# Performance work log

Hardware: AMD Instinct MI355X
Metric: run time of the kernel (lower is better)

Reference implementation:

```python
import jax, jax.numpy as jnp
import numpy as np

B, C, H, W = 2, 256, 64, 64
NUM_HEADS = 4
HEAD_DIM = C // NUM_HEADS
N = H * W


def setup_inputs() -> dict:
    key = jax.random.key(0)
    ks = jax.random.split(key, 10)
    x = jax.random.normal(ks[0], (B, C, H, W), dtype=jnp.float32)
    # mostly-True mask; diagonal forced True so every row has a valid key
    m = jax.random.uniform(ks[1], (B, N, N)) > 0.1
    spatial_mask = m | jnp.eye(N, dtype=bool)[None]
    s = 1.0 / np.sqrt(C)
    wq = jax.random.normal(ks[2], (C, C), dtype=jnp.float32) * s
    bq = jnp.zeros((C,), jnp.float32)
    wk = jax.random.normal(ks[3], (C, C), dtype=jnp.float32) * s
    bk = jnp.zeros((C,), jnp.float32)
    wv = jax.random.normal(ks[4], (C, C), dtype=jnp.float32) * s
    bv = jnp.zeros((C,), jnp.float32)
    # torch zero-inits out_proj; use random weights for a non-trivial baseline
    wo = jax.random.normal(ks[5], (C, C), dtype=jnp.float32) * s
    bo = jnp.zeros((C,), jnp.float32)
    return {"x": x, "spatial_mask": spatial_mask, "wq": wq, "bq": bq,
            "wk": wk, "bk": bk, "wv": wv, "bv": bv, "wo": wo, "bo": bo}


def reference(x, spatial_mask, wq, bq, wk, bk, wv, bv, wo, bo):
    b, c, h, w = x.shape
    n = h * w
    nh, hd = NUM_HEADS, HEAD_DIM
    scale = hd ** -0.5
    x_flat = x.reshape(b, c, n).transpose(0, 2, 1)           # [b, n, c]
    q = (x_flat @ wq.T + bq).reshape(b, n, nh, hd).transpose(0, 2, 1, 3)
    k = (x_flat @ wk.T + bk).reshape(b, n, nh, hd).transpose(0, 2, 1, 3)
    v = (x_flat @ wv.T + bv).reshape(b, n, nh, hd).transpose(0, 2, 1, 3)
    logits = jnp.einsum('bhqd,bhkd->bhqk', q, k) * scale      # [b, nh, n, n]
    logits = jnp.where(spatial_mask[:, None], logits, -jnp.inf)
    attn = jax.nn.softmax(logits, axis=-1)                    # dropout = identity (eval)
    out = jnp.einsum('bhqk,bhkd->bhqd', attn, v)              # [b, nh, n, hd]
    out = out.transpose(0, 2, 1, 3).reshape(b, n, c)
    out = out @ wo.T + bo
    return out.transpose(0, 2, 1).reshape(b, c, h, w)
```

## Files before the change

### kernel.cpp

```cpp
#include <hip/hip_runtime.h>
#include <math.h>

namespace {
constexpr int B_    = 2;
constexpr int C_    = 256;
constexpr int NHEAD = 4;
constexpr int HDIM  = 64;
constexpr int NTOK  = 4096;
constexpr float SCALE = 0.125f;
constexpr float LOG2E = 1.44269504f;
}

typedef _Float16 half8  __attribute__((ext_vector_type(8)));
typedef _Float16 half4  __attribute__((ext_vector_type(4)));
typedef __fp16   fp16x2 __attribute__((ext_vector_type(2)));
typedef float    floatx4 __attribute__((ext_vector_type(4)));

__global__ __launch_bounds__(256) void pack_mask(
    const unsigned int* __restrict__ m32, unsigned int* __restrict__ packed)
{
    int c0 = 0, c1 = 0, c2 = 0, c3 = 0;
    #pragma unroll
    for (int i = 0; i < 16; i++) {
        const unsigned int d = m32[i];
        c0 += (d == 0x00000001u);
        c1 += (d == 0x3F803F80u);
        c2 += (d == 0x3F800000u);
        c3 += (d == 0x01010101u);
    }
    int fmt = 1, best = c1;
    if (c0 > best) { best = c0; fmt = 0; }
    if (c2 > best) { best = c2; fmt = 2; }
    if (c3 > best) { best = c3; fmt = 3; }

    const unsigned int W = blockIdx.x * 256 + threadIdx.x;
    unsigned int bits = 0;
    if (fmt == 1) {
        const uint4* p4 = (const uint4*)(m32 + (size_t)W * 16);
        #pragma unroll
        for (int i = 0; i < 4; i++) {
            const uint4 v = p4[i];
            const unsigned int d[4] = { v.x, v.y, v.z, v.w };
            #pragma unroll
            for (int j = 0; j < 4; j++) {
                const int e = i * 8 + j * 2;
                bits |= ((d[j] & 0xFFFFu) ? 1u : 0u) << e;
                bits |= ((d[j] >> 16)     ? 1u : 0u) << (e + 1);
            }
        }
    } else if (fmt != 3) {
        const uint4* p4 = (const uint4*)(m32 + (size_t)W * 32);
        #pragma unroll
        for (int i = 0; i < 8; i++) {
            const uint4 v = p4[i];
            bits |= (v.x ? 1u : 0u) << (i * 4 + 0);
            bits |= (v.y ? 1u : 0u) << (i * 4 + 1);
            bits |= (v.z ? 1u : 0u) << (i * 4 + 2);
            bits |= (v.w ? 1u : 0u) << (i * 4 + 3);
        }
    } else {
        const uint4* p4 = (const uint4*)(m32 + (size_t)W * 8);
        #pragma unroll
        for (int i = 0; i < 2; i++) {
            const uint4 v = p4[i];
            const unsigned int d[4] = { v.x, v.y, v.z, v.w };
            #pragma unroll
            for (int j = 0; j < 4; j++) {
                const int e = (i * 4 + j) * 4;
                bits |= ((d[j] & 0x000000FFu) ? 1u : 0u) << (e + 0);
                bits |= ((d[j] & 0x0000FF00u) ? 1u : 0u) << (e + 1);
                bits |= ((d[j] & 0x00FF0000u) ? 1u : 0u) << (e + 2);
                bits |= ((d[j] & 0xFF000000u) ? 1u : 0u) << (e + 3);
            }
        }
    }
    packed[W] = bits;
}

__global__ __launch_bounds__(256) void qkv_mfma(
    const float* __restrict__ x,
    const float* __restrict__ wq, const float* __restrict__ bq,
    const float* __restrict__ wk, const float* __restrict__ bk,
    const float* __restrict__ wv, const float* __restrict__ bv,
    _Float16* __restrict__ qo, _Float16* __restrict__ ko,
    _Float16* __restrict__ vo)
{
    const int nt = blockIdx.x;
    const int b  = blockIdx.y;
    const int p  = blockIdx.z;

    const float* w; const float* bias;
    if (p == 0)      { w = wq; bias = bq; }
    else if (p == 1) { w = wk; bias = bk; }
    else             { w = wv; bias = bv; }

    const int t    = threadIdx.x;
    const int wid  = t >> 6;
    const int lane = t & 63;
    const int quad = lane >> 4;
    const int l15  = lane & 15;
    const int n0   = nt * 64;

    __shared__ _Float16 xsh[64 * 264];
    __shared__ _Float16 wsh[64 * 72];
    __shared__ _Float16 tbuf[64 * 72];

    const int srow = t >> 2;
    const int sc   = (t & 3) * 16;

    {
        const int cr = t >> 4;
        const int nu = (t & 15) * 4;
        const float* xb = x + (size_t)b * C_ * NTOK;
        #pragma unroll
        for (int cc = 0; cc < 16; cc++) {
            const int cl = cc * 16 + cr;
            const float4 v = *(const float4*)&xb[(size_t)cl * NTOK + n0 + nu];
            xsh[(nu + 0) * 264 + cl] = (_Float16)v.x;
            xsh[(nu + 1) * 264 + cl] = (_Float16)v.y;
            xsh[(nu + 2) * 264 + cl] = (_Float16)v.z;
            xsh[(nu + 3) * 264 + cl] = (_Float16)v.w;
        }
    }

    for (int h = 0; h < NHEAD; h++) {
        const int co0 = h * 64;
        floatx4 acc[4];
        #pragma unroll
        for (int i = 0; i < 4; i++) acc[i] = (floatx4)0.f;

        for (int c0 = 0; c0 < C_; c0 += 64) {
            {
                const float* wr = &w[(size_t)(co0 + srow) * C_ + c0 + sc];
                half8 h0, h1;
                #pragma unroll
                for (int u = 0; u < 2; u++) {
                    const float4 a = *(const float4*)&wr[u * 4];
                    h0[u*4+0]=(_Float16)a.x; h0[u*4+1]=(_Float16)a.y;
                    h0[u*4+2]=(_Float16)a.z; h0[u*4+3]=(_Float16)a.w;
                }
                #pragma unroll
                for (int u = 0; u < 2; u++) {
                    const float4 a = *(const float4*)&wr[8 + u * 4];
                    h1[u*4+0]=(_Float16)a.x; h1[u*4+1]=(_Float16)a.y;
                    h1[u*4+2]=(_Float16)a.z; h1[u*4+3]=(_Float16)a.w;
                }
                *(half8*)&wsh[srow * 72 + sc]     = h0;
                *(half8*)&wsh[srow * 72 + sc + 8] = h1;
            }
            __syncthreads();
            const half8 a0 = *(const half8*)&wsh[(wid * 16 + l15) * 72 + quad * 8];
            const half8 a1 = *(const half8*)&wsh[(wid * 16 + l15) * 72 + 32 + quad * 8];
            #pragma unroll
            for (int nt2 = 0; nt2 < 4; nt2++) {
                const half8 b0 = *(const half8*)&xsh[(nt2 * 16 + l15) * 264 + c0 + quad * 8];
                const half8 b1 = *(const half8*)&xsh[(nt2 * 16 + l15) * 264 + c0 + 32 + quad * 8];
                acc[nt2] = __builtin_amdgcn_mfma_f32_16x16x32_f16(a0, b0, acc[nt2], 0, 0, 0);
                acc[nt2] = __builtin_amdgcn_mfma_f32_16x16x32_f16(a1, b1, acc[nt2], 0, 0, 0);
            }
            __syncthreads();
        }

        const float4 bb4 = *(const float4*)&bias[co0 + wid * 16 + quad * 4];
        const float bb[4] = { bb4.x, bb4.y, bb4.z, bb4.w };

        if (p < 2) {
            const float osc = (p == 0) ? (SCALE * LOG2E) : 1.0f;
            #pragma unroll
            for (int nt2 = 0; nt2 < 4; nt2++) {
                half4 hv;
                #pragma unroll
                for (int i = 0; i < 4; i++)
                    hv[i] = (_Float16)((acc[nt2][i] + bb[i]) * osc);
                *(half4*)&tbuf[(nt2 * 16 + l15) * 72 + wid * 16 + quad * 4] = hv;
            }
            __syncthreads();
            _Float16* dh = (p == 0 ? qo : ko) + (size_t)(b * NHEAD + h) * NTOK * HDIM;
            const half8 o0 = *(const half8*)&tbuf[srow * 72 + sc];
            const half8 o1 = *(const half8*)&tbuf[srow * 72 + sc + 8];
            *(half8*)&dh[(size_t)(n0 + srow) * HDIM + sc]     = o0;
            *(half8*)&dh[(size_t)(n0 + srow) * HDIM + sc + 8] = o1;
        } else {
            #pragma unroll
            for (int nt2 = 0; nt2 < 4; nt2++)
                #pragma unroll
                for (int i = 0; i < 4; i++)
                    tbuf[(wid * 16 + quad * 4 + i) * 72 + nt2 * 16 + l15] =
                        (_Float16)(acc[nt2][i] + bb[i]);
            __syncthreads();
            _Float16* vth = vo + (size_t)(b * NHEAD + h) * HDIM * NTOK;
            const half8 o0 = *(const half8*)&tbuf[srow * 72 + sc];
            const half8 o1 = *(const half8*)&tbuf[srow * 72 + sc + 8];
            *(half8*)&vth[(size_t)srow * NTOK + n0 + sc]     = o0;
            *(half8*)&vth[(size_t)srow * NTOK + n0 + sc + 8] = o1;
        }
        __syncthreads();
    }
}

__global__ __launch_bounds__(512) void attn(
    const _Float16* __restrict__ q, const _Float16* __restrict__ k,
    const _Float16* __restrict__ vt, const unsigned int* __restrict__ mpacked,
    _Float16* __restrict__ ao)
{
    const int b  = blockIdx.z;
    const int h  = blockIdx.y;
    const int q0 = blockIdx.x * 64;
    const int t    = threadIdx.x;
    const int w    = t >> 6;
    const int lane = t & 63;
    const int quad = lane >> 4;
    const int l15  = lane & 15;
    const int half = w >> 2;
    const int w4   = w & 3;
    const int koff = half * (NTOK / 2);

    __shared__ __align__(16) _Float16 ksA[64 * 72];
    __shared__ __align__(16) _Float16 vsA[64 * 72];
    __shared__ __align__(16) _Float16 psA[64 * 72];
    __shared__ __align__(16) _Float16 ksB[64 * 72];
    __shared__ __align__(16) _Float16 vsB[64 * 72];
    __shared__ __align__(16) _Float16 psB[64 * 72];

    _Float16* ksc = half ? ksB : ksA;
    _Float16* vsc = half ? vsB : vsA;
    _Float16* ps  = half ? psB : psA;

    const size_t head_off = (size_t)(b * NHEAD + h) * NTOK * HDIM;
    const _Float16* qb  = q  + head_off;
    const _Float16* kb  = k  + head_off;
    const _Float16* vtb = vt + head_off;
    const unsigned int* mrow = mpacked + (size_t)b * NTOK * 128;

    const int qrow = q0 + w4 * 16 + l15;
    half8 aq0 = *(const half8*)&qb[(size_t)qrow * HDIM + quad * 8];
    half8 aq1 = *(const half8*)&qb[(size_t)qrow * HDIM + 32 + quad * 8];
    const unsigned int* mq = &mrow[(size_t)qrow * 128];

    const int tl   = t & 255;
    const int srow = tl >> 2;
    const int scol = (tl & 3) * 16;

    half8 kreg0 = *(const half8*)&kb[(size_t)(koff + srow) * HDIM + scol];
    half8 kreg1 = *(const half8*)&kb[(size_t)(koff + srow) * HDIM + scol + 8];
    half8 vreg0 = *(const half8*)&vtb[(size_t)srow * NTOK + koff + scol];
    half8 vreg1 = *(const half8*)&vtb[(size_t)srow * NTOK + koff + scol + 8];

    uint2 mw = *(const uint2*)&mq[koff >> 5];
    uint2 mw_nxt = mw;

    float l_loc = 0.f;
    floatx4 o_acc[4];
    #pragma unroll
    for (int i = 0; i < 4; i++) o_acc[i] = (floatx4)0.f;

    _Float16* psrow = &ps[(w4 * 16 + l15) * 72];

    for (int kt = 0; kt < NTOK / 128; kt++) {
        const int k0 = koff + kt * 64;
        __syncthreads();
        *(half8*)&ksc[srow * 72 + scol]     = kreg0;
        *(half8*)&ksc[srow * 72 + scol + 8] = kreg1;
        *(half8*)&vsc[srow * 72 + scol]     = vreg0;
        *(half8*)&vsc[srow * 72 + scol + 8] = vreg1;
        __syncthreads();

        if (kt + 1 < NTOK / 128) {
            kreg0 = *(const half8*)&kb[(size_t)(k0 + 64 + srow) * HDIM + scol];
            kreg1 = *(const half8*)&kb[(size_t)(k0 + 64 + srow) * HDIM + scol + 8];
            vreg0 = *(const half8*)&vtb[(size_t)srow * NTOK + k0 + 64 + scol];
            vreg1 = *(const half8*)&vtb[(size_t)srow * NTOK + k0 + 64 + scol + 8];
            mw_nxt = *(const uint2*)&mq[(k0 + 64) >> 5];
        }

        floatx4 sa[4];
        __builtin_amdgcn_s_setprio(1);
        #pragma unroll
        for (int ct = 0; ct < 4; ct++) {
            sa[ct] = (floatx4)0.f;
            const half8 ka0 = *(const half8*)&ksc[(ct * 16 + l15) * 72 + quad * 8];
            const half8 ka1 = *(const half8*)&ksc[(ct * 16 + l15) * 72 + 32 + quad * 8];
            sa[ct] = __builtin_amdgcn_mfma_f32_16x16x32_f16(ka0, aq0, sa[ct], 0, 0, 0);
            sa[ct] = __builtin_amdgcn_mfma_f32_16x16x32_f16(ka1, aq1, sa[ct], 0, 0, 0);
        }
        __builtin_amdgcn_s_setprio(0);

        #pragma unroll
        for (int ct = 0; ct < 4; ct++) {
            const unsigned int word = (ct < 2) ? mw.x : mw.y;
            const unsigned nib = (word >> (((ct & 1) << 4) + quad * 4)) & 0xFu;
            const float p0 = __builtin_amdgcn_exp2f((nib & 1u) ? sa[ct][0] : -3.0e38f);
            const float p1 = __builtin_amdgcn_exp2f((nib & 2u) ? sa[ct][1] : -3.0e38f);
            const float p2 = __builtin_amdgcn_exp2f((nib & 4u) ? sa[ct][2] : -3.0e38f);
            const float p3 = __builtin_amdgcn_exp2f((nib & 8u) ? sa[ct][3] : -3.0e38f);
            l_loc += (p0 + p1) + (p2 + p3);
            const fp16x2 lo = __builtin_amdgcn_cvt_pkrtz(p0, p1);
            const fp16x2 hi = __builtin_amdgcn_cvt_pkrtz(p2, p3);
            half4 pv;
            pv[0] = (_Float16)lo[0]; pv[1] = (_Float16)lo[1];
            pv[2] = (_Float16)hi[0]; pv[3] = (_Float16)hi[1];
            *(half4*)&psrow[ct * 16 + quad * 4] = pv;
        }
        mw = mw_nxt;

        const half8 pb0 = *(const half8*)&psrow[quad * 8];
        const half8 pb1 = *(const half8*)&psrow[32 + quad * 8];
        __builtin_amdgcn_s_setprio(1);
        #pragma unroll
        for (int dt = 0; dt < 4; dt++) {
            const half8 va0 = *(const half8*)&vsc[(dt * 16 + l15) * 72 + quad * 8];
            const half8 va1 = *(const half8*)&vsc[(dt * 16 + l15) * 72 + 32 + quad * 8];
            o_acc[dt] = __builtin_amdgcn_mfma_f32_16x16x32_f16(va0, pb0, o_acc[dt], 0, 0, 0);
            o_acc[dt] = __builtin_amdgcn_mfma_f32_16x16x32_f16(va1, pb1, o_acc[dt], 0, 0, 0);
        }
        __builtin_amdgcn_s_setprio(0);
    }

    l_loc += __shfl_xor(l_loc, 16, 64);
    l_loc += __shfl_xor(l_loc, 32, 64);

    __syncthreads();
    float* oex = (float*)ksA;
    float* lex = (float*)vsA;
    if (w >= 4) {
        float* dst = &oex[((size_t)(w - 4) * 64 + lane) * 16];
        #pragma unroll
        for (int dt = 0; dt < 4; dt++)
            *(floatx4*)&dst[dt * 4] = o_acc[dt];
        if (quad == 0) lex[(w - 4) * 16 + l15] = l_loc;
    }
    __syncthreads();
    if (w < 4) {
        const float* src = &oex[((size_t)w * 64 + lane) * 16];
        const float lt = l_loc + lex[w * 16 + l15];
        const float inv = (lt > 0.f) ? (1.0f / lt) : 0.f;
        _Float16* aob = ao + ((size_t)b * NTOK + q0 + w * 16 + l15) * C_ + h * 64;
        #pragma unroll
        for (int dt = 0; dt < 4; dt++) {
            const floatx4 o2 = *(const floatx4*)&src[dt * 4];
            half4 r;
            #pragma unroll
            for (int rr = 0; rr < 4; rr++)
                r[rr] = (_Float16)((o_acc[dt][rr] + o2[rr]) * inv);
            *(half4*)&aob[dt * 16 + quad * 4] = r;
        }
    }
}

__global__ __launch_bounds__(256) void out_mfma(
    const _Float16* __restrict__ ao, const float* __restrict__ wo,
    const float* __restrict__ bo, float* __restrict__ out)
{
    const int nt  = blockIdx.x;
    const int cot = blockIdx.y;
    const int b   = blockIdx.z;
    const int t    = threadIdx.x;
    const int wid  = t >> 6;
    const int lane = t & 63;
    const int quad = lane >> 4;
    const int l15  = lane & 15;
    const int n0  = nt * 64;
    const int co0 = cot * 64;

    __shared__ _Float16 wsh[64 * 72];
    __shared__ _Float16 ash[64 * 72];
    __shared__ float    tf[64 * 68];

    const int srow = t >> 2;
    const int sc   = (t & 3) * 16;

    floatx4 acc[4];
    #pragma unroll
    for (int i = 0; i < 4; i++) acc[i] = (floatx4)0.f;

    const _Float16* aob = ao + ((size_t)b * NTOK + n0) * C_;

    for (int c0 = 0; c0 < C_; c0 += 64) {
        {
            const float* wr = &wo[(size_t)(co0 + srow) * C_ + c0 + sc];
            half8 h0, h1;
            #pragma unroll
            for (int u = 0; u < 2; u++) {
                const float4 a = *(const float4*)&wr[u * 4];
                h0[u*4+0]=(_Float16)a.x; h0[u*4+1]=(_Float16)a.y;
                h0[u*4+2]=(_Float16)a.z; h0[u*4+3]=(_Float16)a.w;
            }
            #pragma unroll
            for (int u = 0; u < 2; u++) {
                const float4 a = *(const float4*)&wr[8 + u * 4];
                h1[u*4+0]=(_Float16)a.x; h1[u*4+1]=(_Float16)a.y;
                h1[u*4+2]=(_Float16)a.z; h1[u*4+3]=(_Float16)a.w;
            }
            *(half8*)&wsh[srow * 72 + sc]     = h0;
            *(half8*)&wsh[srow * 72 + sc + 8] = h1;
        }
        {
            const _Float16* ar = &aob[(size_t)srow * C_ + c0 + sc];
            *(half8*)&ash[srow * 72 + sc]     = *(const half8*)&ar[0];
            *(half8*)&ash[srow * 72 + sc + 8] = *(const half8*)&ar[8];
        }
        __syncthreads();
        const half8 a0 = *(const half8*)&wsh[(wid * 16 + l15) * 72 + quad * 8];
        const half8 a1 = *(const half8*)&wsh[(wid * 16 + l15) * 72 + 32 + quad * 8];
        #pragma unroll
        for (int nt2 = 0; nt2 < 4; nt2++) {
            const half8 b0 = *(const half8*)&ash[(nt2 * 16 + l15) * 72 + quad * 8];
            const half8 b1 = *(const half8*)&ash[(nt2 * 16 + l15) * 72 + 32 + quad * 8];
            acc[nt2] = __builtin_amdgcn_mfma_f32_16x16x32_f16(a0, b0, acc[nt2], 0, 0, 0);
            acc[nt2] = __builtin_amdgcn_mfma_f32_16x16x32_f16(a1, b1, acc[nt2], 0, 0, 0);
        }
        __syncthreads();
    }

    #pragma unroll
    for (int nt2 = 0; nt2 < 4; nt2++)
        #pragma unroll
        for (int i = 0; i < 4; i++)
            tf[(wid * 16 + quad * 4 + i) * 68 + nt2 * 16 + l15] = acc[nt2][i];
    __syncthreads();

    const int row = t >> 2;
    const int c4  = (t & 3) * 16;
    const float bb = bo[co0 + row];
    float* orow = &out[((size_t)(b * C_ + co0 + row)) * NTOK + n0 + c4];
    #pragma unroll
    for (int u = 0; u < 4; u++) {
        float4 v = *(const float4*)&tf[row * 68 + c4 + u * 4];
        v.x += bb; v.y += bb; v.z += bb; v.w += bb;
        *(float4*)&orow[u * 4] = v;
    }
}

extern "C" void kernel_launch(void* const* d_in, const int* in_sizes, int n_in,
                              void* d_out, int out_size, void* d_ws, size_t ws_size,
                              hipStream_t stream) {
    const float* x    = (const float*)d_in[0];
    const void*  mask = d_in[1];
    const float* wq   = (const float*)d_in[2];
    const float* bq   = (const float*)d_in[3];
    const float* wk   = (const float*)d_in[4];
    const float* bk   = (const float*)d_in[5];
    const float* wv   = (const float*)d_in[6];
    const float* bv   = (const float*)d_in[7];
    const float* wo   = (const float*)d_in[8];
    const float* bo   = (const float*)d_in[9];
    float* out = (float*)d_out;

    const size_t qkv_elems = (size_t)B_ * NHEAD * NTOK * HDIM;
    _Float16* wsh = (_Float16*)d_ws;
    _Float16* qbuf  = wsh;
    _Float16* kbuf  = wsh + qkv_elems;
    _Float16* vtbuf = wsh + 2 * qkv_elems;
    _Float16* aobuf = wsh + 3 * qkv_elems;
    unsigned int* mpacked = (unsigned int*)(wsh + 4 * qkv_elems);

    pack_mask<<<dim3((B_ * NTOK * 128) / 256), 256, 0, stream>>>(
        (const unsigned int*)mask, mpacked);
    qkv_mfma<<<dim3(NTOK / 64, B_, 3), 256, 0, stream>>>(
        x, wq, bq, wk, bk, wv, bv, qbuf, kbuf, vtbuf);
    attn<<<dim3(NTOK / 64, NHEAD, B_), 512, 0, stream>>>(
        qbuf, kbuf, vtbuf, mpacked, aobuf);
    out_mfma<<<dim3(NTOK / 64, C_ / 64, B_), 256, 0, stream>>>(
        aobuf, wo, bo, out);
}
```

Baseline: 307.0 us.

## Double-buffer K/V tiles in LDS and keep P in registers via permlane swaps

The attention loop now ping-pongs between two LDS buffers for K and V, so the next tile is written after the PV MFMAs and each iteration needs one barrier instead of two. The softmax probabilities no longer round-trip through an LDS P tile. They are rearranged into the MFMA B-operand layout in registers using v_permlane32_swap and v_permlane16_swap, which removes LDS writes and reads and frees LDS space. The risk is whether the permlane shuffle exactly reproduces the old P layout, plus the larger unrolled code and the inline-asm fallback with s_nops.

```diff
diff --git a/kernel.cpp b/kernel.cpp
--- a/kernel.cpp
+++ b/kernel.cpp
@@ -15,6 +15,27 @@
 typedef _Float16 half4  __attribute__((ext_vector_type(4)));
 typedef __fp16   fp16x2 __attribute__((ext_vector_type(2)));
 typedef float    floatx4 __attribute__((ext_vector_type(4)));
+typedef int      int4v   __attribute__((ext_vector_type(4)));
+typedef unsigned int uint2v __attribute__((ext_vector_type(2)));
+
+__device__ __forceinline__ void plswap32(int &a, int &b) {
+#if __has_builtin(__builtin_amdgcn_permlane32_swap)
+    const uint2v r = __builtin_amdgcn_permlane32_swap((unsigned)a, (unsigned)b, false, false);
+    a = (int)r[0]; b = (int)r[1];
+#else
+    asm volatile("s_nop 1\n\tv_permlane32_swap_b32 %0, %1\n\ts_nop 1"
+                 : "+v"(a), "+v"(b));
+#endif
+}
+__device__ __forceinline__ void plswap16(int &a, int &b) {
+#if __has_builtin(__builtin_amdgcn_permlane16_swap)
+    const uint2v r = __builtin_amdgcn_permlane16_swap((unsigned)a, (unsigned)b, false, false);
+    a = (int)r[0]; b = (int)r[1];
+#else
+    asm volatile("s_nop 1\n\tv_permlane16_swap_b32 %0, %1\n\ts_nop 1"
+                 : "+v"(a), "+v"(b));
+#endif
+}
 
 __global__ __launch_bounds__(256) void pack_mask(
     const unsigned int* __restrict__ m32, unsigned int* __restrict__ packed)
@@ -215,16 +236,8 @@
     const int w4   = w & 3;
     const int koff = half * (NTOK / 2);
 
-    __shared__ __align__(16) _Float16 ksA[64 * 72];
-    __shared__ __align__(16) _Float16 vsA[64 * 72];
-    __shared__ __align__(16) _Float16 psA[64 * 72];
-    __shared__ __align__(16) _Float16 ksB[64 * 72];
-    __shared__ __align__(16) _Float16 vsB[64 * 72];
-    __shared__ __align__(16) _Float16 psB[64 * 72];
-
-    _Float16* ksc = half ? ksB : ksA;
-    _Float16* vsc = half ? vsB : vsA;
-    _Float16* ps  = half ? psB : psA;
+    __shared__ __align__(16) char smem_raw[2 * 4 * 64 * 72 * 2];
+    _Float16* const sbase = (_Float16*)(smem_raw + half * 36864);
 
     const size_t head_off = (size_t)(b * NHEAD + h) * NTOK * HDIM;
     const _Float16* qb  = q  + head_off;
@@ -254,74 +267,92 @@
     #pragma unroll
     for (int i = 0; i < 4; i++) o_acc[i] = (floatx4)0.f;
 
-    _Float16* psrow = &ps[(w4 * 16 + l15) * 72];
-
-    for (int kt = 0; kt < NTOK / 128; kt++) {
-        const int k0 = koff + kt * 64;
-        __syncthreads();
-        *(half8*)&ksc[srow * 72 + scol]     = kreg0;
-        *(half8*)&ksc[srow * 72 + scol + 8] = kreg1;
-        *(half8*)&vsc[srow * 72 + scol]     = vreg0;
-        *(half8*)&vsc[srow * 72 + scol + 8] = vreg1;
-        __syncthreads();
-
-        if (kt + 1 < NTOK / 128) {
-            kreg0 = *(const half8*)&kb[(size_t)(k0 + 64 + srow) * HDIM + scol];
-            kreg1 = *(const half8*)&kb[(size_t)(k0 + 64 + srow) * HDIM + scol + 8];
-            vreg0 = *(const half8*)&vtb[(size_t)srow * NTOK + k0 + 64 + scol];
-            vreg1 = *(const half8*)&vtb[(size_t)srow * NTOK + k0 + 64 + scol + 8];
-            mw_nxt = *(const uint2*)&mq[(k0 + 64) >> 5];
-        }
-
-        floatx4 sa[4];
-        __builtin_amdgcn_s_setprio(1);
-        #pragma unroll
-        for (int ct = 0; ct < 4; ct++) {
-            sa[ct] = (floatx4)0.f;
-            const half8 ka0 = *(const half8*)&ksc[(ct * 16 + l15) * 72 + quad * 8];
-            const half8 ka1 = *(const half8*)&ksc[(ct * 16 + l15) * 72 + 32 + quad * 8];
-            sa[ct] = __builtin_amdgcn_mfma_f32_16x16x32_f16(ka0, aq0, sa[ct], 0, 0, 0);
-            sa[ct] = __builtin_amdgcn_mfma_f32_16x16x32_f16(ka1, aq1, sa[ct], 0, 0, 0);
-        }
-        __builtin_amdgcn_s_setprio(0);
-
-        #pragma unroll
-        for (int ct = 0; ct < 4; ct++) {
-            const unsigned int word = (ct < 2) ? mw.x : mw.y;
-            const unsigned nib = (word >> (((ct & 1) << 4) + quad * 4)) & 0xFu;
-            const float p0 = __builtin_amdgcn_exp2f((nib & 1u) ? sa[ct][0] : -3.0e38f);
-            const float p1 = __builtin_amdgcn_exp2f((nib & 2u) ? sa[ct][1] : -3.0e38f);
-            const float p2 = __builtin_amdgcn_exp2f((nib & 4u) ? sa[ct][2] : -3.0e38f);
-            const float p3 = __builtin_amdgcn_exp2f((nib & 8u) ? sa[ct][3] : -3.0e38f);
-            l_loc += (p0 + p1) + (p2 + p3);
-            const fp16x2 lo = __builtin_amdgcn_cvt_pkrtz(p0, p1);
-            const fp16x2 hi = __builtin_amdgcn_cvt_pkrtz(p2, p3);
-            half4 pv;
-            pv[0] = (_Float16)lo[0]; pv[1] = (_Float16)lo[1];
-            pv[2] = (_Float16)hi[0]; pv[3] = (_Float16)hi[1];
-            *(half4*)&psrow[ct * 16 + quad * 4] = pv;
-        }
-        mw = mw_nxt;
-
-        const half8 pb0 = *(const half8*)&psrow[quad * 8];
-        const half8 pb1 = *(const half8*)&psrow[32 + quad * 8];
-        __builtin_amdgcn_s_setprio(1);
-        #pragma unroll
-        for (int dt = 0; dt < 4; dt++) {
-            const half8 va0 = *(const half8*)&vsc[(dt * 16 + l15) * 72 + quad * 8];
-            const half8 va1 = *(const half8*)&vsc[(dt * 16 + l15) * 72 + 32 + quad * 8];
-            o_acc[dt] = __builtin_amdgcn_mfma_f32_16x16x32_f16(va0, pb0, o_acc[dt], 0, 0, 0);
-            o_acc[dt] = __builtin_amdgcn_mfma_f32_16x16x32_f16(va1, pb1, o_acc[dt], 0, 0, 0);
-        }
-        __builtin_amdgcn_s_setprio(0);
-    }
+    *(half8*)&sbase[srow * 72 + scol]            = kreg0;
+    *(half8*)&sbase[srow * 72 + scol + 8]        = kreg1;
+    *(half8*)&sbase[4608 + srow * 72 + scol]     = vreg0;
+    *(half8*)&sbase[4608 + srow * 72 + scol + 8] = vreg1;
+    __syncthreads();
+
+#define SOFTMAX_CT(CT, WORD, SH, Pa, Pb)                                          \
+    {                                                                             \
+        const unsigned nib = ((WORD) >> ((SH) + quad * 4)) & 0xFu;                \
+        const float p0 = __builtin_amdgcn_exp2f((nib & 1u) ? sa[CT][0] : -3.0e38f);\
+        const float p1 = __builtin_amdgcn_exp2f((nib & 2u) ? sa[CT][1] : -3.0e38f);\
+        const float p2 = __builtin_amdgcn_exp2f((nib & 4u) ? sa[CT][2] : -3.0e38f);\
+        const float p3 = __builtin_amdgcn_exp2f((nib & 8u) ? sa[CT][3] : -3.0e38f);\
+        l_loc += (p0 + p1) + (p2 + p3);                                           \
+        Pa = __builtin_bit_cast(int, __builtin_amdgcn_cvt_pkrtz(p0, p1));         \
+        Pb = __builtin_bit_cast(int, __builtin_amdgcn_cvt_pkrtz(p2, p3));         \
+    }
+
+#define ATTN_TILE(RO, WO, KT, PF)                                                 \
+    {                                                                             \
+        if (PF) {                                                                 \
+            const int k0n = koff + (KT) * 64 + 64;                                \
+            kreg0 = *(const half8*)&kb[(size_t)(k0n + srow) * HDIM + scol];       \
+            kreg1 = *(const half8*)&kb[(size_t)(k0n + srow) * HDIM + scol + 8];   \
+            vreg0 = *(const half8*)&vtb[(size_t)srow * NTOK + k0n + scol];        \
+            vreg1 = *(const half8*)&vtb[(size_t)srow * NTOK + k0n + scol + 8];    \
+            mw_nxt = *(const uint2*)&mq[k0n >> 5];                                \
+        }                                                                         \
+        floatx4 sa[4];                                                            \
+        __builtin_amdgcn_s_setprio(1);                                            \
+        _Pragma("unroll")                                                         \
+        for (int ct = 0; ct < 4; ct++) {                                          \
+            sa[ct] = (floatx4)0.f;                                                \
+            const half8 ka0 = *(const half8*)&sbase[(RO) + (ct*16 + l15)*72 + quad*8];      \
+            const half8 ka1 = *(const half8*)&sbase[(RO) + (ct*16 + l15)*72 + 32 + quad*8]; \
+            sa[ct] = __builtin_amdgcn_mfma_f32_16x16x32_f16(ka0, aq0, sa[ct], 0, 0, 0);     \
+            sa[ct] = __builtin_amdgcn_mfma_f32_16x16x32_f16(ka1, aq1, sa[ct], 0, 0, 0);     \
+        }                                                                         \
+        __builtin_amdgcn_s_setprio(0);                                            \
+        int P00, P01, P10, P11, P20, P21, P30, P31;                               \
+        SOFTMAX_CT(0, mw.x, 0,  P00, P01)                                         \
+        SOFTMAX_CT(1, mw.x, 16, P10, P11)                                         \
+        SOFTMAX_CT(2, mw.y, 0,  P20, P21)                                         \
+        SOFTMAX_CT(3, mw.y, 16, P30, P31)                                         \
+        mw = mw_nxt;                                                              \
+                                                   \
+        plswap32(P00, P10); plswap32(P01, P11);                                   \
+        plswap32(P20, P30); plswap32(P21, P31);                                   \
+                                               \
+        plswap16(P00, P10); plswap16(P01, P11);                                   \
+        plswap16(P20, P30); plswap16(P21, P31);                                   \
+        const half8 pb0 = __builtin_bit_cast(half8, (int4v){P00, P01, P10, P11}); \
+        const half8 pb1 = __builtin_bit_cast(half8, (int4v){P20, P21, P30, P31}); \
+        __builtin_amdgcn_s_setprio(1);                                            \
+        _Pragma("unroll")                                                         \
+        for (int dt = 0; dt < 4; dt++) {                                          \
+            const half8 va0 = *(const half8*)&sbase[(RO) + 4608 + (dt*16 + l15)*72 + quad*8];      \
+            const half8 va1 = *(const half8*)&sbase[(RO) + 4608 + (dt*16 + l15)*72 + 32 + quad*8]; \
+            o_acc[dt] = __builtin_amdgcn_mfma_f32_16x16x32_f16(va0, pb0, o_acc[dt], 0, 0, 0);      \
+            o_acc[dt] = __builtin_amdgcn_mfma_f32_16x16x32_f16(va1, pb1, o_acc[dt], 0, 0, 0);      \
+        }                                                                         \
+        __builtin_amdgcn_s_setprio(0);                                            \
+        if (PF) {                                                                 \
+            *(half8*)&sbase[(WO) + srow * 72 + scol]            = kreg0;          \
+            *(half8*)&sbase[(WO) + srow * 72 + scol + 8]        = kreg1;          \
+            *(half8*)&sbase[(WO) + 4608 + srow * 72 + scol]     = vreg0;          \
+            *(half8*)&sbase[(WO) + 4608 + srow * 72 + scol + 8] = vreg1;          \
+        }                                                                         \
+        __syncthreads();                                                          \
+    }
+
+    for (int kt2 = 0; kt2 < 15; kt2++) {
+        ATTN_TILE(0,    9216, 2 * kt2,     1)
+        ATTN_TILE(9216, 0,    2 * kt2 + 1, 1)
+    }
+    ATTN_TILE(0,    9216, 30, 1)
+    ATTN_TILE(9216, 0,    31, 0)
+
+#undef ATTN_TILE
+#undef SOFTMAX_CT
 
     l_loc += __shfl_xor(l_loc, 16, 64);
     l_loc += __shfl_xor(l_loc, 32, 64);
 
-    __syncthreads();
-    float* oex = (float*)ksA;
-    float* lex = (float*)vsA;
+    float* oex = (float*)smem_raw;
+    float* lex = (float*)(smem_raw + 16384);
     if (w >= 4) {
         float* dst = &oex[((size_t)(w - 4) * 64 + lane) * 16];
         #pragma unroll
```

New measurement: 298.6 us. -2.7%, faster.
